# Performance work log

Measured on AMD Instinct MI355X. Metric: run time of the kernel, lower is better.

## Reference

```python
import jax, jax.numpy as jnp
import numpy as np
from jax import lax

WINDOW_SIZE = 11
SIGMA = 1.5
DATA_RANGE = 1.0
EPS = 1e-8


def _gauss_1d(window_size=WINDOW_SIZE, sigma=SIGMA):
    coords = jnp.arange(window_size, dtype=jnp.float32) - window_size // 2
    g = jnp.exp(-(coords ** 2) / (2.0 * sigma ** 2))
    return g / g.sum()


def _gaussian_filter(x, w1d):
    # Separable depthwise blur: horizontal then vertical, VALID padding (use_padding=False).
    C = x.shape[1]
    win = w1d.shape[0]
    kh = jnp.broadcast_to(w1d.reshape(1, 1, 1, win), (C, 1, 1, win))  # OIHW, groups=C
    kv = jnp.broadcast_to(w1d.reshape(1, 1, win, 1), (C, 1, win, 1))
    dn = ('NCHW', 'OIHW', 'NCHW')
    out = lax.conv_general_dilated(x, kh, (1, 1), 'VALID',
                                   dimension_numbers=dn, feature_group_count=C)
    out = lax.conv_general_dilated(out, kv, (1, 1), 'VALID',
                                   dimension_numbers=dn, feature_group_count=C)
    return out


def setup_inputs() -> dict:
    key = jax.random.key(0)
    k1, k2 = jax.random.split(key)
    B, C, H, W = 16, 3, 768, 768
    X = jax.random.uniform(k1, (B, C, H, W), dtype=jnp.float32)
    Y = jax.random.uniform(k2, (B, C, H, W), dtype=jnp.float32)
    window = _gauss_1d()
    return {"X": X, "Y": Y, "window": window}


def reference(X, Y, window):
    K1, K2 = 0.01, 0.03
    C1 = (K1 * DATA_RANGE) ** 2
    C2 = (K2 * DATA_RANGE) ** 2
    mu_x = _gaussian_filter(X, window)
    mu_y = _gaussian_filter(Y, window)
    sigma_x = _gaussian_filter(X * X, window) - mu_x ** 2
    sigma_y = _gaussian_filter(Y * Y, window) - mu_y ** 2
    sigma_xy = _gaussian_filter(X * Y, window) - mu_x * mu_y
    cs = (2.0 * sigma_xy + C2) / (sigma_x + sigma_y + C2 + EPS)
    cs = jax.nn.relu(cs)
    ssim_map = (2.0 * mu_x * mu_y + C1) / (mu_x ** 2 + mu_y ** 2 + C1 + EPS) * cs
    ssim_val = ssim_map.mean(axis=(1, 2, 3))  # [B]
    return ssim_val
```

## Files before the change

kernel.cpp:

```cpp
#include <hip/hip_runtime.h>


typedef float f32x2 __attribute__((ext_vector_type(2)));

#define H_IMG 768
#define W_IMG 768
#define OH 758
#define OW_TOT 758
#define OWS 256
#define NSEG 16

static __device__ __forceinline__ f32x2 mk2(float a, float b) {
    f32x2 r; r.x = a; r.y = b; return r;
}

struct RowRegs {
    float4 xa, xb, xc, ya, yb, yc;
    float2 xd, yd;
};

static __device__ __forceinline__ void load_rows(RowRegs& rr,
        const float* __restrict__ xr, const float* __restrict__ yr,
        int k0, int k1, int k2, int k3) {
    rr.xa = *(const float4*)(xr + k0);
    rr.xb = *(const float4*)(xr + k1);
    rr.xc = *(const float4*)(xr + k2);
    rr.xd = *(const float2*)(xr + k3);
    rr.ya = *(const float4*)(yr + k0);
    rr.yb = *(const float4*)(yr + k1);
    rr.yc = *(const float4*)(yr + k2);
    rr.yd = *(const float2*)(yr + k3);
}

__global__ void ssim_zero_out(float* __restrict__ out) {
    if (threadIdx.x < 16) out[threadIdx.x] = 0.0f;
}

__attribute__((amdgpu_flat_work_group_size(256, 256), amdgpu_waves_per_eu(3, 3)))
__global__ void ssim_fused(const float* __restrict__ X, const float* __restrict__ Y,
                           const float* __restrict__ Wg, float* __restrict__ out) {
    const float C1 = 1e-4f, C2 = 9e-4f, EPS = 1e-8f;
    const float INV_COUNT = 1.0f / (3.0f * 758.0f * 758.0f);

    const int t = threadIdx.x;
    int bx = blockIdx.x;
    const int seg = bx & (NSEG - 1); bx >>= 4;
    const int strip = bx % 3; bx /= 3;
    const int ch = bx % 3;
    const int b  = bx / 3;

    const int R0 = (OH * seg) / NSEG;
    const int Rend = (OH * (seg + 1)) / NSEG;
    const int hseg = Rend - R0;
    const int c0 = strip * OWS;

    const float* Xi = X + (size_t)(b * 3 + ch) * (H_IMG * W_IMG);
    const float* Yi = Y + (size_t)(b * 3 + ch) * (H_IMG * W_IMG);

    f32x2 ww[11];
#pragma unroll
    for (int k = 0; k < 11; ++k) { float wk = Wg[k]; ww[k] = mk2(wk, wk); }

    __shared__ float hb[2][4][4][OWS];
    __shared__ float red[4];

    const int sA = t >> 6;
    const int cg = t & 63;
    const int colbase = c0 + 4 * cg;
    const int k0 = min(colbase,      W_IMG - 4);
    const int k1 = min(colbase + 4,  W_IMG - 4);
    const int k2 = min(colbase + 8,  W_IMG - 4);
    const int k3 = min(colbase + 12, W_IMG - 2);

    f32x2 rg01[16], rg23[16];
#pragma unroll
    for (int j = 0; j < 16; ++j) { rg01[j] = mk2(0.f, 0.f); rg23[j] = mk2(0.f, 0.f); }

    const bool colok = (c0 + t) < OW_TOT;
    float local = 0.0f;
    const int M = (hseg + 13) >> 2;

    RowRegs r0, r1;
    {
        int rr = min(R0 + sA, H_IMG - 1);
        load_rows(r0, Xi + (size_t)rr * W_IMG, Yi + (size_t)rr * W_IMG, k0, k1, k2, k3);
    }

    for (int mb = 0; mb < M; mb += 4) {
#pragma unroll
        for (int p = 0; p < 4; ++p) {
            const int m = mb + p;
            if (m < M) {
                const int pb = p & 1;
                RowRegs& cur = pb ? r1 : r0;
                RowRegs& nxt = pb ? r0 : r1;

                if (m + 1 < M) {
                    int rn = R0 + 4 * (m + 1) + sA;
                    rn = min(rn, H_IMG - 1);
                    load_rows(nxt, Xi + (size_t)rn * W_IMG, Yi + (size_t)rn * W_IMG,
                              k0, k1, k2, k3);
                }

                {
                    f32x2 v[14] = {
                        mk2(cur.xa.x, cur.ya.x), mk2(cur.xa.y, cur.ya.y),
                        mk2(cur.xa.z, cur.ya.z), mk2(cur.xa.w, cur.ya.w),
                        mk2(cur.xb.x, cur.yb.x), mk2(cur.xb.y, cur.yb.y),
                        mk2(cur.xb.z, cur.yb.z), mk2(cur.xb.w, cur.yb.w),
                        mk2(cur.xc.x, cur.yc.x), mk2(cur.xc.y, cur.yc.y),
                        mk2(cur.xc.z, cur.yc.z), mk2(cur.xc.w, cur.yc.w),
                        mk2(cur.xd.x, cur.yd.x), mk2(cur.xd.y, cur.yd.y)};

                    {
                        f32x2 hm[4];
#pragma unroll
                        for (int cc = 0; cc < 4; ++cc) {
                            f32x2 a = mk2(0.f, 0.f);
#pragma unroll
                            for (int k = 0; k < 11; ++k)
                                a = __builtin_elementwise_fma(ww[k], v[cc + k], a);
                            hm[cc] = a;
                        }
                        *(float4*)&hb[pb][sA][0][4 * cg] = make_float4(hm[0].x, hm[1].x, hm[2].x, hm[3].x);
                        *(float4*)&hb[pb][sA][1][4 * cg] = make_float4(hm[0].y, hm[1].y, hm[2].y, hm[3].y);
                    }
#pragma unroll
                    for (int j = 0; j < 14; ++j) {
                        const float xx = v[j].x, yy = v[j].y;
                        v[j] = mk2(fmaf(xx, xx, yy * yy), xx * yy);
                    }
                    {
                        f32x2 hs[4];
#pragma unroll
                        for (int cc = 0; cc < 4; ++cc) {
                            f32x2 a = mk2(0.f, 0.f);
#pragma unroll
                            for (int k = 0; k < 11; ++k)
                                a = __builtin_elementwise_fma(ww[k], v[cc + k], a);
                            hs[cc] = a;
                        }
                        *(float4*)&hb[pb][sA][2][4 * cg] = make_float4(hs[0].x, hs[1].x, hs[2].x, hs[3].x);
                        *(float4*)&hb[pb][sA][3][4 * cg] = make_float4(hs[0].y, hs[1].y, hs[2].y, hs[3].y);
                    }
                }
                __syncthreads();

                {
#pragma unroll
                    for (int s2 = 0; s2 < 4; ++s2) {
                        const int sl = (4 * p + s2) & 15;
                        rg01[sl] = mk2(hb[pb][s2][0][t], hb[pb][s2][1][t]);
                        rg23[sl] = mk2(hb[pb][s2][2][t], hb[pb][s2][3][t]);
                    }
                    if (m >= 2) {
#pragma unroll
                        for (int s2 = 0; s2 < 4; ++s2) {
                            const int orel = 4 * m - 10 + s2;
                            f32x2 a01 = mk2(0.f, 0.f), a23 = mk2(0.f, 0.f);
#pragma unroll
                            for (int k = 0; k < 11; ++k) {
                                const int sl = (4 * p + s2 + k + 6) & 15;
                                a01 = __builtin_elementwise_fma(ww[k], rg01[sl], a01);
                                a23 = __builtin_elementwise_fma(ww[k], rg23[sl], a23);
                            }
                            const float a0 = a01.x, a1 = a01.y, a2 = a23.x, a3 = a23.y;
                            const float mux2 = a0 * a0;
                            const float muy2 = a1 * a1;
                            const float mxy  = a0 * a1;
                            const float sigsum = a2 - mux2 - muy2;
                            const float sxy    = a3 - mxy;
                            const float num = (2.0f * mxy + C1) * (2.0f * sxy + C2);
                            const float den = (mux2 + muy2 + C1 + EPS) * (sigsum + C2 + EPS);
                            const float v = fmaxf(__fdividef(num, den), 0.0f);
                            if (colok && (orel >= 0) && (orel < hseg)) local += v;
                        }
                    }
                }
            }
        }
    }

    float v = local;
#pragma unroll
    for (int off = 32; off > 0; off >>= 1) v += __shfl_down(v, off, 64);
    if ((t & 63) == 0) red[t >> 6] = v;
    __syncthreads();
    if (t == 0) {
        atomicAdd(&out[b], (red[0] + red[1] + red[2] + red[3]) * INV_COUNT);
    }
}

extern "C" void kernel_launch(void* const* d_in, const int* in_sizes, int n_in,
                              void* d_out, int out_size, void* d_ws, size_t ws_size,
                              hipStream_t stream) {
    const float* X  = (const float*)d_in[0];
    const float* Y  = (const float*)d_in[1];
    const float* Wg = (const float*)d_in[2];
    float* out = (float*)d_out;

    hipLaunchKernelGGL(ssim_zero_out, dim3(1), dim3(64), 0, stream, out);
    hipLaunchKernelGGL(ssim_fused, dim3(16 * 3 * 3 * NSEG), dim3(256), 0, stream,
                       X, Y, Wg, out);
}
```

Before: 276.6 us.

## Remap threads so LDS exchange is intra-wave and drop block barriers

The thread-to-work mapping changes so that each group of four adjacent lanes handles the four rows of one column quad. Every horizontal-pass value a thread reads back from LDS was then written by a lane in its own wavefront. This lets the per-iteration __syncthreads be replaced by an lgkmcnt wait plus a compiler fence, and the LDS buffer shrinks to a single padded copy with a 260-float row stride. The trade-off is that global loads are now spread across four rows per lane group, which may hurt coalescing, and correctness depends on in-order LDS execution within a wavefront.

```diff
diff --git a/kernel.cpp b/kernel.cpp
--- a/kernel.cpp
+++ b/kernel.cpp
@@ -9,6 +9,10 @@
 #define OW_TOT 758
 #define OWS 256
 #define NSEG 16
+#define LSTR 260
+
+#define WAIT_LDS() asm volatile("s_waitcnt lgkmcnt(0)" ::: "memory")
+#define FENCE_C()  asm volatile("" ::: "memory")
 
 static __device__ __forceinline__ f32x2 mk2(float a, float b) {
     f32x2 r; r.x = a; r.y = b; return r;
@@ -61,11 +65,11 @@
 #pragma unroll
     for (int k = 0; k < 11; ++k) { float wk = Wg[k]; ww[k] = mk2(wk, wk); }
 
-    __shared__ float hb[2][4][4][OWS];
+    __shared__ float hb[4][4][LSTR];
     __shared__ float red[4];
 
-    const int sA = t >> 6;
-    const int cg = t & 63;
+    const int sA = t & 3;
+    const int cg = t >> 2;
     const int colbase = c0 + 4 * cg;
     const int k0 = min(colbase,      W_IMG - 4);
     const int k1 = min(colbase + 4,  W_IMG - 4);
@@ -91,9 +95,9 @@
         for (int p = 0; p < 4; ++p) {
             const int m = mb + p;
             if (m < M) {
-                const int pb = p & 1;
-                RowRegs& cur = pb ? r1 : r0;
-                RowRegs& nxt = pb ? r0 : r1;
+                const int pr = p & 1;
+                RowRegs& cur = pr ? r1 : r0;
+                RowRegs& nxt = pr ? r0 : r1;
 
                 if (m + 1 < M) {
                     int rn = R0 + 4 * (m + 1) + sA;
@@ -122,8 +126,8 @@
                                 a = __builtin_elementwise_fma(ww[k], v[cc + k], a);
                             hm[cc] = a;
                         }
-                        *(float4*)&hb[pb][sA][0][4 * cg] = make_float4(hm[0].x, hm[1].x, hm[2].x, hm[3].x);
-                        *(float4*)&hb[pb][sA][1][4 * cg] = make_float4(hm[0].y, hm[1].y, hm[2].y, hm[3].y);
+                        *(float4*)&hb[0][sA][4 * cg] = make_float4(hm[0].x, hm[1].x, hm[2].x, hm[3].x);
+                        *(float4*)&hb[1][sA][4 * cg] = make_float4(hm[0].y, hm[1].y, hm[2].y, hm[3].y);
                     }
 #pragma unroll
                     for (int j = 0; j < 14; ++j) {
@@ -140,18 +144,18 @@
                                 a = __builtin_elementwise_fma(ww[k], v[cc + k], a);
                             hs[cc] = a;
                         }
-                        *(float4*)&hb[pb][sA][2][4 * cg] = make_float4(hs[0].x, hs[1].x, hs[2].x, hs[3].x);
-                        *(float4*)&hb[pb][sA][3][4 * cg] = make_float4(hs[0].y, hs[1].y, hs[2].y, hs[3].y);
+                        *(float4*)&hb[2][sA][4 * cg] = make_float4(hs[0].x, hs[1].x, hs[2].x, hs[3].x);
+                        *(float4*)&hb[3][sA][4 * cg] = make_float4(hs[0].y, hs[1].y, hs[2].y, hs[3].y);
                     }
                 }
-                __syncthreads();
+                WAIT_LDS();
 
                 {
 #pragma unroll
                     for (int s2 = 0; s2 < 4; ++s2) {
                         const int sl = (4 * p + s2) & 15;
-                        rg01[sl] = mk2(hb[pb][s2][0][t], hb[pb][s2][1][t]);
-                        rg23[sl] = mk2(hb[pb][s2][2][t], hb[pb][s2][3][t]);
+                        rg01[sl] = mk2(hb[0][s2][t], hb[1][s2][t]);
+                        rg23[sl] = mk2(hb[2][s2][t], hb[3][s2][t]);
                     }
                     if (m >= 2) {
 #pragma unroll
@@ -177,6 +181,7 @@
                         }
                     }
                 }
+                FENCE_C();
             }
         }
     }
```

After: 289.1 us. 4.5% more time.
